# Kernel optimization log

Hardware: AMD Instinct MI355X
Metric: run time of the kernel (lower is better)

The kernel has to match this reference:

```python
import jax, jax.numpy as jnp
import numpy as np

N = 500_000      # nodes
B = 8192         # graphs
F = 128          # num_node_features
C = 128          # channels (num_out_features)
EPS = 1e-16      # matches torch_geometric.utils.softmax denominator eps


def setup_inputs() -> dict:
    key = jax.random.key(0)
    ks = jax.random.split(key, 16)
    w = lambda k, shape: jax.random.normal(k, shape, dtype=jnp.float32) * 0.02
    inp = {
        "x": jax.random.normal(ks[0], (N, F), dtype=jnp.float32),
        "u": jax.random.normal(ks[1], (B, C), dtype=jnp.float32),
        "batch": jnp.sort(jax.random.randint(ks[2], (N,), 0, B, dtype=jnp.int32)),
        "size": B,
        # gate_nn: Linear(C,C) -> ReLU -> Linear(C,1)
        "gate_w1": w(ks[3], (C, C)), "gate_b1": w(ks[4], (C,)),
        "gate_w2": w(ks[5], (C, 1)), "gate_b2": w(ks[6], (1,)),
        # node_nn: Linear(F,C) -> ReLU -> Linear(C,C)
        "node_w1": w(ks[7], (F, C)), "node_b1": w(ks[8], (C,)),
        "node_w2": w(ks[9], (C, C)), "node_b2": w(ks[10], (C,)),
        # ques_nn: Linear(C,C) -> ReLU -> Linear(C,C)
        "ques_w1": w(ks[11], (C, C)), "ques_b1": w(ks[12], (C,)),
        "ques_w2": w(ks[13], (C, C)), "ques_b2": w(ks[14], (C,)),
    }
    return inp


def _mlp2(x, w1, b1, w2, b2):
    return jax.nn.relu(x @ w1 + b1) @ w2 + b2


def reference(x, u, batch, size,
              gate_w1, gate_b1, gate_w2, gate_b2,
              node_w1, node_b1, node_w2, node_b2,
              ques_w1, ques_b1, ques_w2, ques_b2):
    # node features h_theta(x): [N, C]
    h = _mlp2(x, node_w1, node_b1, node_w2, node_b2)
    # question features per graph, gathered to nodes: [N, C]
    q = _mlp2(u, ques_w1, ques_b1, ques_w2, ques_b2)
    # gate scores: [N, 1]
    gate = _mlp2(q[batch] * h, gate_w1, gate_b1, gate_w2, gate_b2)
    # segment softmax over graphs (torch_geometric.utils.softmax)
    m = jax.ops.segment_max(gate, batch, num_segments=size)          # [B, 1]
    m = jnp.where(jnp.isfinite(m), m, 0.0)                            # empty segments
    e = jnp.exp(gate - m[batch])                                      # [N, 1]
    s = jax.ops.segment_sum(e, batch, num_segments=size)              # [B, 1]
    alpha = e / (s[batch] + EPS)                                      # [N, 1]
    # scatter_add pooling: [B, C]
    out = jax.ops.segment_sum(alpha * h, batch, num_segments=size)
    return out
```

## Files before the change

kernel.cpp:

```cpp
#include <hip/hip_runtime.h>
#include <math.h>

#define NN 500000
#define NB 8192
#define GMAX 16

typedef _Float16 f16x8 __attribute__((ext_vector_type(8)));
typedef __fp16 fp16x2 __attribute__((ext_vector_type(2)));
typedef float f32x4 __attribute__((ext_vector_type(4)));

__device__ inline f16x8 cvt8(float4 a, float4 b) {
    union { fp16x2 p[4]; f16x8 r; } u;
    u.p[0] = __builtin_amdgcn_cvt_pkrtz(a.x, a.y);
    u.p[1] = __builtin_amdgcn_cvt_pkrtz(a.z, a.w);
    u.p[2] = __builtin_amdgcn_cvt_pkrtz(b.x, b.y);
    u.p[3] = __builtin_amdgcn_cvt_pkrtz(b.z, b.w);
    return u.r;
}

__global__ void prep_w(const float* __restrict__ nw1, const float* __restrict__ nw2,
                       const float* __restrict__ gw1, const float* __restrict__ gw2,
                       const float* __restrict__ qw1, const float* __restrict__ qw2,
                       _Float16* __restrict__ wT1, _Float16* __restrict__ wT2,
                       _Float16* __restrict__ wTg, _Float16* __restrict__ wTq1,
                       _Float16* __restrict__ wTq2, _Float16* __restrict__ g2h) {
    int k = blockIdx.x;
    int n = threadIdx.x;
    wT1[n * 128 + k]  = (_Float16)nw1[k * 128 + n];
    wT2[n * 128 + k]  = (_Float16)nw2[k * 128 + n];
    wTg[n * 128 + k]  = (_Float16)gw1[k * 128 + n];
    wTq1[n * 128 + k] = (_Float16)qw1[k * 128 + n];
    wTq2[n * 128 + k] = (_Float16)qw2[k * 128 + n];
    if (k == 0) g2h[n] = (_Float16)gw2[n];
}

__launch_bounds__(512, 4)
__global__ void q_kernel(const float* __restrict__ u,
                         const _Float16* __restrict__ wTq1, const _Float16* __restrict__ wTq2,
                         const float* __restrict__ qb1, const float* __restrict__ qb2,
                         _Float16* __restrict__ q, float* __restrict__ Ppre, float* __restrict__ s) {
    __shared__ __align__(16) _Float16 tbuf[128][136];
    const int tid  = threadIdx.x;
    const int wave = tid >> 6;
    const int lane = tid & 63;
    const int lrow = lane & 15;
    const int quad = lane >> 4;
    const int wr   = wave >> 1;
    const int wc   = wave & 1;
    const int row0 = blockIdx.x * 128;
    const int rbase = wr * 32;

    for (int idx = tid; idx < 128 * 128; idx += 512) Ppre[(size_t)row0 * 128 + idx] = 0.f;
    if (tid < 128) s[row0 + tid] = 0.f;

    f32x4 acc[2][4];
    const f32x4 fz = {0.f, 0.f, 0.f, 0.f};
#pragma unroll
    for (int mi = 0; mi < 2; ++mi)
#pragma unroll
        for (int ci = 0; ci < 4; ++ci) acc[mi][ci] = fz;

#pragma unroll
    for (int ki = 0; ki < 4; ++ki) {
        const int k = ki * 32 + quad * 8;
        f16x8 a[2];
#pragma unroll
        for (int mi = 0; mi < 2; ++mi) {
            int r = row0 + rbase + mi * 16 + lrow;
            const float4* up = (const float4*)(u + (size_t)r * 128 + k);
            a[mi] = cvt8(up[0], up[1]);
        }
        f16x8 b[4];
#pragma unroll
        for (int ci = 0; ci < 4; ++ci)
            b[ci] = *(const f16x8*)(wTq1 + (size_t)(wc * 64 + ci * 16 + lrow) * 128 + k);
#pragma unroll
        for (int mi = 0; mi < 2; ++mi)
#pragma unroll
            for (int ci = 0; ci < 4; ++ci)
                acc[mi][ci] = __builtin_amdgcn_mfma_f32_16x16x32_f16(a[mi], b[ci], acc[mi][ci], 0, 0, 0);
    }
#pragma unroll
    for (int ci = 0; ci < 4; ++ci) {
        int c = wc * 64 + ci * 16 + lrow;
        float bv = qb1[c];
#pragma unroll
        for (int mi = 0; mi < 2; ++mi)
#pragma unroll
            for (int i = 0; i < 4; ++i) {
                int r = rbase + mi * 16 + quad * 4 + i;
                tbuf[r][c] = (_Float16)fmaxf(acc[mi][ci][i] + bv, 0.f);
            }
    }
    __syncthreads();

#pragma unroll
    for (int mi = 0; mi < 2; ++mi)
#pragma unroll
        for (int ci = 0; ci < 4; ++ci) acc[mi][ci] = fz;
#pragma unroll
    for (int ki = 0; ki < 4; ++ki) {
        const int k = ki * 32 + quad * 8;
        f16x8 a[2];
#pragma unroll
        for (int mi = 0; mi < 2; ++mi)
            a[mi] = *(const f16x8*)&tbuf[rbase + mi * 16 + lrow][k];
        f16x8 b[4];
#pragma unroll
        for (int ci = 0; ci < 4; ++ci)
            b[ci] = *(const f16x8*)(wTq2 + (size_t)(wc * 64 + ci * 16 + lrow) * 128 + k);
#pragma unroll
        for (int mi = 0; mi < 2; ++mi)
#pragma unroll
            for (int ci = 0; ci < 4; ++ci)
                acc[mi][ci] = __builtin_amdgcn_mfma_f32_16x16x32_f16(a[mi], b[ci], acc[mi][ci], 0, 0, 0);
    }
#pragma unroll
    for (int ci = 0; ci < 4; ++ci) {
        int c = wc * 64 + ci * 16 + lrow;
        float bv = qb2[c];
#pragma unroll
        for (int mi = 0; mi < 2; ++mi)
#pragma unroll
            for (int i = 0; i < 4; ++i) {
                int r = row0 + rbase + mi * 16 + quad * 4 + i;
                q[(size_t)r * 128 + c] = (_Float16)(acc[mi][ci][i] + bv);
            }
    }
}

__launch_bounds__(256, 4)
__global__ void hg_kernel(const float* __restrict__ x, const int* __restrict__ batch,
                          const _Float16* __restrict__ qglob,
                          const _Float16* __restrict__ wT1, const _Float16* __restrict__ wT2,
                          const _Float16* __restrict__ wTg, const _Float16* __restrict__ g2h,
                          const float* __restrict__ nb1, const float* __restrict__ nb2,
                          const float* __restrict__ gb1, const float* __restrict__ gb2,
                          float* __restrict__ Ppre, float* __restrict__ s) {
    __shared__ __align__(16) _Float16 t1buf[64][136];
    __shared__ __align__(16) _Float16 scratch[64][136];
    __shared__ __align__(16) _Float16 qsE[GMAX][136];
    __shared__ float gpart[2][64];
    __shared__ float sacc[GMAX];
    __shared__ int batch_t[64];
    __shared__ int maxrel_sh;

    const int tid  = threadIdx.x;
    const int wave = tid >> 6;
    const int lane = tid & 63;
    const int lrow = lane & 15;
    const int quad = lane >> 4;
    const int wr   = wave >> 1;
    const int wc   = wave & 1;
    const int row0 = blockIdx.x * 64;
    const int rbase = wr * 32;

    float4 xraw[4][2][2];
#pragma unroll
    for (int ki = 0; ki < 4; ++ki)
#pragma unroll
        for (int mi = 0; mi < 2; ++mi) {
            int r = min(row0 + rbase + mi * 16 + lrow, NN - 1);
            const float4* xp = (const float4*)(x + (size_t)r * 128 + ki * 32 + quad * 8);
            xraw[ki][mi][0] = xp[0];
            xraw[ki][mi][1] = xp[1];
        }

    if (wave == 0) {
        int bv = batch[min(row0 + lane, NN - 1)];
        batch_t[lane] = bv;
        int b0 = __shfl(bv, 0, 64);
        int rel = bv - b0;
#pragma unroll
        for (int off = 32; off >= 1; off >>= 1) rel = max(rel, __shfl_xor(rel, off, 64));
        if (lane == 0) maxrel_sh = rel;
    }
    __syncthreads();
    const int b_lo = batch_t[0];
    const int gcnt = min(maxrel_sh + 1, GMAX);

    for (int idx = tid; idx < gcnt * 16; idx += 256)
        *(f16x8*)&qsE[idx >> 4][(idx & 15) * 8] =
            *(const f16x8*)(qglob + (size_t)(b_lo + (idx >> 4)) * 128 + (idx & 15) * 8);

    int grel[2][4];
#pragma unroll
    for (int mi = 0; mi < 2; ++mi)
#pragma unroll
        for (int i = 0; i < 4; ++i)
            grel[mi][i] = batch_t[rbase + mi * 16 + quad * 4 + i] - b_lo;

    f16x8 a16[4][2];
#pragma unroll
    for (int ki = 0; ki < 4; ++ki)
#pragma unroll
        for (int mi = 0; mi < 2; ++mi)
            a16[ki][mi] = cvt8(xraw[ki][mi][0], xraw[ki][mi][1]);

    f32x4 acc[2][4];
    const f32x4 fz = {0.f, 0.f, 0.f, 0.f};
#pragma unroll
    for (int mi = 0; mi < 2; ++mi)
#pragma unroll
        for (int ci = 0; ci < 4; ++ci) acc[mi][ci] = fz;

#pragma unroll
    for (int ki = 0; ki < 4; ++ki) {
        const int k = ki * 32 + quad * 8;
        f16x8 b[4];
#pragma unroll
        for (int ci = 0; ci < 4; ++ci)
            b[ci] = *(const f16x8*)(wT1 + (size_t)(wc * 64 + ci * 16 + lrow) * 128 + k);
#pragma unroll
        for (int mi = 0; mi < 2; ++mi)
#pragma unroll
            for (int ci = 0; ci < 4; ++ci)
                acc[mi][ci] = __builtin_amdgcn_mfma_f32_16x16x32_f16(a16[ki][mi], b[ci], acc[mi][ci], 0, 0, 0);
    }
#pragma unroll
    for (int ci = 0; ci < 4; ++ci) {
        int c = wc * 64 + ci * 16 + lrow;
        float bv = nb1[c];
#pragma unroll
        for (int mi = 0; mi < 2; ++mi)
#pragma unroll
            for (int i = 0; i < 4; ++i) {
                int r = rbase + mi * 16 + quad * 4 + i;
                t1buf[r][c] = (_Float16)fmaxf(acc[mi][ci][i] + bv, 0.f);
            }
    }
    __syncthreads();

#pragma unroll
    for (int mi = 0; mi < 2; ++mi)
#pragma unroll
        for (int ci = 0; ci < 4; ++ci) acc[mi][ci] = fz;
#pragma unroll
    for (int ki = 0; ki < 4; ++ki) {
        const int k = ki * 32 + quad * 8;
        f16x8 a[2];
#pragma unroll
        for (int mi = 0; mi < 2; ++mi)
            a[mi] = *(const f16x8*)&t1buf[rbase + mi * 16 + lrow][k];
        f16x8 b[4];
#pragma unroll
        for (int ci = 0; ci < 4; ++ci)
            b[ci] = *(const f16x8*)(wT2 + (size_t)(wc * 64 + ci * 16 + lrow) * 128 + k);
#pragma unroll
        for (int mi = 0; mi < 2; ++mi)
#pragma unroll
            for (int ci = 0; ci < 4; ++ci)
                acc[mi][ci] = __builtin_amdgcn_mfma_f32_16x16x32_f16(a[mi], b[ci], acc[mi][ci], 0, 0, 0);
    }
#pragma unroll
    for (int ci = 0; ci < 4; ++ci) {
        int c = wc * 64 + ci * 16 + lrow;
        float bv = nb2[c];
#pragma unroll
        for (int mi = 0; mi < 2; ++mi)
#pragma unroll
            for (int i = 0; i < 4; ++i) {
                int r = rbase + mi * 16 + quad * 4 + i;
                float h = acc[mi][ci][i] + bv;
                int g = grel[mi][i];
                float qv = (g < GMAX) ? (float)qsE[g][c]
                                      : (float)qglob[(size_t)(b_lo + g) * 128 + c];
                scratch[r][c] = (_Float16)(qv * h);
            }
    }
    __syncthreads();

    for (int idx = tid; idx < GMAX * 136 / 2; idx += 256) ((float*)qsE)[idx] = 0.f;
    if (tid < GMAX) sacc[tid] = 0.f;

#pragma unroll
    for (int mi = 0; mi < 2; ++mi)
#pragma unroll
        for (int ci = 0; ci < 4; ++ci) acc[mi][ci] = fz;
    float g2hreg[4];
#pragma unroll
    for (int ci = 0; ci < 4; ++ci) g2hreg[ci] = (float)g2h[wc * 64 + ci * 16 + lrow];
#pragma unroll
    for (int ki = 0; ki < 4; ++ki) {
        const int k = ki * 32 + quad * 8;
        f16x8 a[2];
#pragma unroll
        for (int mi = 0; mi < 2; ++mi)
            a[mi] = *(const f16x8*)&scratch[rbase + mi * 16 + lrow][k];
        f16x8 b[4];
#pragma unroll
        for (int ci = 0; ci < 4; ++ci)
            b[ci] = *(const f16x8*)(wTg + (size_t)(wc * 64 + ci * 16 + lrow) * 128 + k);
#pragma unroll
        for (int mi = 0; mi < 2; ++mi)
#pragma unroll
            for (int ci = 0; ci < 4; ++ci)
                acc[mi][ci] = __builtin_amdgcn_mfma_f32_16x16x32_f16(a[mi], b[ci], acc[mi][ci], 0, 0, 0);
    }
    float p[2][4] = {{0.f, 0.f, 0.f, 0.f}, {0.f, 0.f, 0.f, 0.f}};
#pragma unroll
    for (int ci = 0; ci < 4; ++ci) {
        int c = wc * 64 + ci * 16 + lrow;
        float bv = gb1[c];
        float w = g2hreg[ci];
#pragma unroll
        for (int mi = 0; mi < 2; ++mi)
#pragma unroll
            for (int i = 0; i < 4; ++i)
                p[mi][i] = fmaf(fmaxf(acc[mi][ci][i] + bv, 0.f), w, p[mi][i]);
    }
#pragma unroll
    for (int off = 1; off <= 8; off <<= 1)
#pragma unroll
        for (int mi = 0; mi < 2; ++mi)
#pragma unroll
            for (int i = 0; i < 4; ++i)
                p[mi][i] += __shfl_xor(p[mi][i], off, 64);
    if (lrow == 0) {
#pragma unroll
        for (int mi = 0; mi < 2; ++mi)
#pragma unroll
            for (int i = 0; i < 4; ++i)
                gpart[wc][rbase + mi * 16 + quad * 4 + i] = p[mi][i];
    }
    __syncthreads();

    const float gb2v = gb2[0];
    if (tid < 64) {
        int r = tid;
        int g = batch_t[r] - b_lo;
        bool valid = (row0 + r) < NN;
        float e = valid ? __expf(gpart[0][r] + gpart[1][r] + gb2v) : 0.f;
        if (g < GMAX) {
            qsE[g][r] = (_Float16)e;
            atomicAdd(&sacc[g], e);
        } else if (valid) {
            atomicAdd(&s[b_lo + g], e);
            for (int c = 0; c < 128; ++c)
                atomicAdd(&Ppre[(size_t)(b_lo + g) * 128 + c], e * (float)t1buf[r][c]);
        }
    }
    __syncthreads();

    f16x8 aE[2];
#pragma unroll
    for (int ki = 0; ki < 2; ++ki)
        aE[ki] = *(const f16x8*)&qsE[lrow][ki * 32 + quad * 8];
    f32x4 pacc[2] = {fz, fz};
#pragma unroll
    for (int ci2 = 0; ci2 < 2; ++ci2) {
        int col = wave * 32 + ci2 * 16 + lrow;
#pragma unroll
        for (int ki = 0; ki < 2; ++ki) {
            f16x8 bh;
#pragma unroll
            for (int j = 0; j < 8; ++j) bh[j] = t1buf[ki * 32 + quad * 8 + j][col];
            pacc[ci2] = __builtin_amdgcn_mfma_f32_16x16x32_f16(aE[ki], bh, pacc[ci2], 0, 0, 0);
        }
    }
#pragma unroll
    for (int ci2 = 0; ci2 < 2; ++ci2)
#pragma unroll
        for (int i = 0; i < 4; ++i) {
            int g = quad * 4 + i;
            if (g < gcnt)
                atomicAdd(&Ppre[(size_t)(b_lo + g) * 128 + wave * 32 + ci2 * 16 + lrow], pacc[ci2][i]);
        }
    if (tid < gcnt) atomicAdd(&s[b_lo + tid], sacc[tid]);
}

__launch_bounds__(512, 4)
__global__ void fin_kernel(const float* __restrict__ Ppre, const float* __restrict__ s,
                           const _Float16* __restrict__ wT2, const float* __restrict__ nb2,
                           float* __restrict__ out) {
    const int tid  = threadIdx.x;
    const int wave = tid >> 6;
    const int lane = tid & 63;
    const int lrow = lane & 15;
    const int quad = lane >> 4;
    const int wr   = wave >> 1;
    const int wc   = wave & 1;
    const int row0 = blockIdx.x * 128;
    const int rbase = wr * 32;

    f32x4 acc[2][4];
    const f32x4 fz = {0.f, 0.f, 0.f, 0.f};
#pragma unroll
    for (int mi = 0; mi < 2; ++mi)
#pragma unroll
        for (int ci = 0; ci < 4; ++ci) acc[mi][ci] = fz;
#pragma unroll
    for (int ki = 0; ki < 4; ++ki) {
        const int k = ki * 32 + quad * 8;
        f16x8 a[2];
#pragma unroll
        for (int mi = 0; mi < 2; ++mi) {
            int r = row0 + rbase + mi * 16 + lrow;
            const float4* pp = (const float4*)(Ppre + (size_t)r * 128 + k);
            a[mi] = cvt8(pp[0], pp[1]);
        }
        f16x8 b[4];
#pragma unroll
        for (int ci = 0; ci < 4; ++ci)
            b[ci] = *(const f16x8*)(wT2 + (size_t)(wc * 64 + ci * 16 + lrow) * 128 + k);
#pragma unroll
        for (int mi = 0; mi < 2; ++mi)
#pragma unroll
            for (int ci = 0; ci < 4; ++ci)
                acc[mi][ci] = __builtin_amdgcn_mfma_f32_16x16x32_f16(a[mi], b[ci], acc[mi][ci], 0, 0, 0);
    }
    float sv[2][4], rinv[2][4];
#pragma unroll
    for (int mi = 0; mi < 2; ++mi)
#pragma unroll
        for (int i = 0; i < 4; ++i) {
            int r = row0 + rbase + mi * 16 + quad * 4 + i;
            sv[mi][i] = s[r];
            rinv[mi][i] = 1.f / (sv[mi][i] + 1e-16f);
        }
#pragma unroll
    for (int ci = 0; ci < 4; ++ci) {
        int c = wc * 64 + ci * 16 + lrow;
        float bv = nb2[c];
#pragma unroll
        for (int mi = 0; mi < 2; ++mi)
#pragma unroll
            for (int i = 0; i < 4; ++i) {
                int r = row0 + rbase + mi * 16 + quad * 4 + i;
                out[(size_t)r * 128 + c] = (acc[mi][ci][i] + sv[mi][i] * bv) * rinv[mi][i];
            }
    }
}

extern "C" void kernel_launch(void* const* d_in, const int* in_sizes, int n_in,
                              void* d_out, int out_size, void* d_ws, size_t ws_size,
                              hipStream_t stream) {
    const float* x    = (const float*)d_in[0];
    const float* u    = (const float*)d_in[1];
    const int* batch  = (const int*)d_in[2];
    const float* gw1  = (const float*)d_in[4];
    const float* gb1  = (const float*)d_in[5];
    const float* gw2  = (const float*)d_in[6];
    const float* gb2  = (const float*)d_in[7];
    const float* nw1  = (const float*)d_in[8];
    const float* nb1  = (const float*)d_in[9];
    const float* nw2  = (const float*)d_in[10];
    const float* nb2  = (const float*)d_in[11];
    const float* qw1  = (const float*)d_in[12];
    const float* qb1  = (const float*)d_in[13];
    const float* qw2  = (const float*)d_in[14];
    const float* qb2  = (const float*)d_in[15];

    char* ws = (char*)d_ws;
    _Float16* q   = (_Float16*)ws;
    float* Ppre   = (float*)(ws + 2097152);
    float* s      = (float*)(ws + 6291456);
    _Float16* wT1 = (_Float16*)(ws + 6324224);
    _Float16* wT2  = wT1 + 16384;
    _Float16* wTg  = wT2 + 16384;
    _Float16* wTq1 = wTg + 16384;
    _Float16* wTq2 = wTq1 + 16384;
    _Float16* g2h  = wTq2 + 16384;
    float* out = (float*)d_out;

    hipLaunchKernelGGL(prep_w, dim3(128), dim3(128), 0, stream,
                       nw1, nw2, gw1, gw2, qw1, qw2, wT1, wT2, wTg, wTq1, wTq2, g2h);
    hipLaunchKernelGGL(q_kernel, dim3(NB / 128), dim3(512), 0, stream,
                       u, wTq1, wTq2, qb1, qb2, q, Ppre, s);
    hipLaunchKernelGGL(hg_kernel, dim3((NN + 63) / 64), dim3(256), 0, stream,
                       x, batch, q, wT1, wT2, wTg, g2h, nb1, nb2, gb1, gb2, Ppre, s);
    hipLaunchKernelGGL(fin_kernel, dim3(NB / 128), dim3(512), 0, stream,
                       Ppre, s, wT2, nb2, out);
}
```

Baseline: 555.5 us.

## Make hg_kernel persistent and prefetch next tile's x and batch

Launches hg_kernel on a fixed grid of 1024 blocks that loop over the 64-row tiles with a grid stride, instead of one block per tile. Inside the loop, the next tile's x rows are loaded into registers, and wave 0 reads its batch ids, while the current tile's MLP, gating and pooling run. This is meant to hide global-load latency behind MFMA work and to cut block launch overhead. The cost is fewer resident blocks, so less latency hiding from occupancy, plus extra live registers for the prefetched data.

Result: slower. 890.8 us (+60.4%).

```diff
diff --git a/kernel.cpp b/kernel.cpp
--- a/kernel.cpp
+++ b/kernel.cpp
@@ -4,6 +4,8 @@
 #define NN 500000
 #define NB 8192
 #define GMAX 16
+#define HG_GRID 1024
+#define HG_NT ((NN + 63) / 64)
 
 typedef _Float16 f16x8 __attribute__((ext_vector_type(8)));
 typedef __fp16 fp16x2 __attribute__((ext_vector_type(2)));
@@ -152,221 +154,246 @@
     const int quad = lane >> 4;
     const int wr   = wave >> 1;
     const int wc   = wave & 1;
-    const int row0 = blockIdx.x * 64;
     const int rbase = wr * 32;
+    const int blk  = (int)blockIdx.x;
+
+    const f32x4 fz = {0.f, 0.f, 0.f, 0.f};
 
     float4 xraw[4][2][2];
-#pragma unroll
-    for (int ki = 0; ki < 4; ++ki)
-#pragma unroll
-        for (int mi = 0; mi < 2; ++mi) {
-            int r = min(row0 + rbase + mi * 16 + lrow, NN - 1);
-            const float4* xp = (const float4*)(x + (size_t)r * 128 + ki * 32 + quad * 8);
-            xraw[ki][mi][0] = xp[0];
-            xraw[ki][mi][1] = xp[1];
-        }
-
+    {
+        const int r0 = blk * 64;
+#pragma unroll
+        for (int ki = 0; ki < 4; ++ki)
+#pragma unroll
+            for (int mi = 0; mi < 2; ++mi) {
+                int r = min(r0 + rbase + mi * 16 + lrow, NN - 1);
+                const float4* xp = (const float4*)(x + (size_t)r * 128 + ki * 32 + quad * 8);
+                xraw[ki][mi][0] = xp[0];
+                xraw[ki][mi][1] = xp[1];
+            }
+    }
+    int bv = 0;
     if (wave == 0) {
-        int bv = batch[min(row0 + lane, NN - 1)];
-        batch_t[lane] = bv;
-        int b0 = __shfl(bv, 0, 64);
-        int rel = bv - b0;
-#pragma unroll
-        for (int off = 32; off >= 1; off >>= 1) rel = max(rel, __shfl_xor(rel, off, 64));
-        if (lane == 0) maxrel_sh = rel;
-    }
-    __syncthreads();
-    const int b_lo = batch_t[0];
-    const int gcnt = min(maxrel_sh + 1, GMAX);
-
-    for (int idx = tid; idx < gcnt * 16; idx += 256)
-        *(f16x8*)&qsE[idx >> 4][(idx & 15) * 8] =
-            *(const f16x8*)(qglob + (size_t)(b_lo + (idx >> 4)) * 128 + (idx & 15) * 8);
-
-    int grel[2][4];
-#pragma unroll
-    for (int mi = 0; mi < 2; ++mi)
-#pragma unroll
-        for (int i = 0; i < 4; ++i)
-            grel[mi][i] = batch_t[rbase + mi * 16 + quad * 4 + i] - b_lo;
-
-    f16x8 a16[4][2];
-#pragma unroll
-    for (int ki = 0; ki < 4; ++ki)
-#pragma unroll
-        for (int mi = 0; mi < 2; ++mi)
-            a16[ki][mi] = cvt8(xraw[ki][mi][0], xraw[ki][mi][1]);
-
-    f32x4 acc[2][4];
-    const f32x4 fz = {0.f, 0.f, 0.f, 0.f};
-#pragma unroll
-    for (int mi = 0; mi < 2; ++mi)
-#pragma unroll
-        for (int ci = 0; ci < 4; ++ci) acc[mi][ci] = fz;
-
-#pragma unroll
-    for (int ki = 0; ki < 4; ++ki) {
-        const int k = ki * 32 + quad * 8;
-        f16x8 b[4];
-#pragma unroll
-        for (int ci = 0; ci < 4; ++ci)
-            b[ci] = *(const f16x8*)(wT1 + (size_t)(wc * 64 + ci * 16 + lrow) * 128 + k);
-#pragma unroll
-        for (int mi = 0; mi < 2; ++mi)
+        int i0 = blk * 64 + lane;
+        bv = batch[min(i0, NN - 1)];
+    }
+
+    for (int t = blk; t < HG_NT; t += HG_GRID) {
+        const int row0  = t * 64;
+        const int rown0 = (t + HG_GRID) * 64;
+
+        if (wave == 0) {
+            batch_t[lane] = bv;
+            int b0 = __shfl(bv, 0, 64);
+            int rel = bv - b0;
+#pragma unroll
+            for (int off = 32; off >= 1; off >>= 1) rel = max(rel, __shfl_xor(rel, off, 64));
+            if (lane == 0) maxrel_sh = rel;
+        }
+        __syncthreads();
+        const int b_lo = batch_t[0];
+        const int gcnt = min(maxrel_sh + 1, GMAX);
+
+        if (wave == 0) bv = batch[min(rown0 + lane, NN - 1)];
+
+        for (int idx = tid; idx < gcnt * 16; idx += 256)
+            *(f16x8*)&qsE[idx >> 4][(idx & 15) * 8] =
+                *(const f16x8*)(qglob + (size_t)(b_lo + (idx >> 4)) * 128 + (idx & 15) * 8);
+
+        int grel[2][4];
+#pragma unroll
+        for (int mi = 0; mi < 2; ++mi)
+#pragma unroll
+            for (int i = 0; i < 4; ++i)
+                grel[mi][i] = batch_t[rbase + mi * 16 + quad * 4 + i] - b_lo;
+
+        f16x8 a16[4][2];
+#pragma unroll
+        for (int ki = 0; ki < 4; ++ki)
+#pragma unroll
+            for (int mi = 0; mi < 2; ++mi)
+                a16[ki][mi] = cvt8(xraw[ki][mi][0], xraw[ki][mi][1]);
+
+        f32x4 acc[2][4];
+#pragma unroll
+        for (int mi = 0; mi < 2; ++mi)
+#pragma unroll
+            for (int ci = 0; ci < 4; ++ci) acc[mi][ci] = fz;
+
+#pragma unroll
+        for (int ki = 0; ki < 4; ++ki) {
+            const int k = ki * 32 + quad * 8;
+            f16x8 b[4];
 #pragma unroll
             for (int ci = 0; ci < 4; ++ci)
-                acc[mi][ci] = __builtin_amdgcn_mfma_f32_16x16x32_f16(a16[ki][mi], b[ci], acc[mi][ci], 0, 0, 0);
-    }
-#pragma unroll
-    for (int ci = 0; ci < 4; ++ci) {
-        int c = wc * 64 + ci * 16 + lrow;
-        float bv = nb1[c];
-#pragma unroll
-        for (int mi = 0; mi < 2; ++mi)
+                b[ci] = *(const f16x8*)(wT1 + (size_t)(wc * 64 + ci * 16 + lrow) * 128 + k);
+#pragma unroll
+            for (int mi = 0; mi < 2; ++mi)
+#pragma unroll
+                for (int ci = 0; ci < 4; ++ci)
+                    acc[mi][ci] = __builtin_amdgcn_mfma_f32_16x16x32_f16(a16[ki][mi], b[ci], acc[mi][ci], 0, 0, 0);
+        }
+#pragma unroll
+        for (int ci = 0; ci < 4; ++ci) {
+            int c = wc * 64 + ci * 16 + lrow;
+            float bvv = nb1[c];
+#pragma unroll
+            for (int mi = 0; mi < 2; ++mi)
+#pragma unroll
+                for (int i = 0; i < 4; ++i) {
+                    int r = rbase + mi * 16 + quad * 4 + i;
+                    t1buf[r][c] = (_Float16)fmaxf(acc[mi][ci][i] + bvv, 0.f);
+                }
+        }
+        __syncthreads();
+
+#pragma unroll
+        for (int ki = 0; ki < 4; ++ki)
+#pragma unroll
+            for (int mi = 0; mi < 2; ++mi) {
+                int r = min(rown0 + rbase + mi * 16 + lrow, NN - 1);
+                const float4* xp = (const float4*)(x + (size_t)r * 128 + ki * 32 + quad * 8);
+                xraw[ki][mi][0] = xp[0];
+                xraw[ki][mi][1] = xp[1];
+            }
+
+#pragma unroll
+        for (int mi = 0; mi < 2; ++mi)
+#pragma unroll
+            for (int ci = 0; ci < 4; ++ci) acc[mi][ci] = fz;
+#pragma unroll
+        for (int ki = 0; ki < 4; ++ki) {
+            const int k = ki * 32 + quad * 8;
+            f16x8 a[2];
+#pragma unroll
+            for (int mi = 0; mi < 2; ++mi)
+                a[mi] = *(const f16x8*)&t1buf[rbase + mi * 16 + lrow][k];
+            f16x8 b[4];
+#pragma unroll
+            for (int ci = 0; ci < 4; ++ci)
+                b[ci] = *(const f16x8*)(wT2 + (size_t)(wc * 64 + ci * 16 + lrow) * 128 + k);
+#pragma unroll
+            for (int mi = 0; mi < 2; ++mi)
+#pragma unroll
+                for (int ci = 0; ci < 4; ++ci)
+                    acc[mi][ci] = __builtin_amdgcn_mfma_f32_16x16x32_f16(a[mi], b[ci], acc[mi][ci], 0, 0, 0);
+        }
+#pragma unroll
+        for (int ci = 0; ci < 4; ++ci) {
+            int c = wc * 64 + ci * 16 + lrow;
+            float bvv = nb2[c];
+#pragma unroll
+            for (int mi = 0; mi < 2; ++mi)
+#pragma unroll
+                for (int i = 0; i < 4; ++i) {
+                    int r = rbase + mi * 16 + quad * 4 + i;
+                    float h = acc[mi][ci][i] + bvv;
+                    int g = grel[mi][i];
+                    float qv = (g < GMAX) ? (float)qsE[g][c]
+                                          : (float)qglob[(size_t)(b_lo + g) * 128 + c];
+                    scratch[r][c] = (_Float16)(qv * h);
+                }
+        }
+        __syncthreads();
+
+        for (int idx = tid; idx < GMAX * 136 / 2; idx += 256) ((float*)qsE)[idx] = 0.f;
+        if (tid < GMAX) sacc[tid] = 0.f;
+
+#pragma unroll
+        for (int mi = 0; mi < 2; ++mi)
+#pragma unroll
+            for (int ci = 0; ci < 4; ++ci) acc[mi][ci] = fz;
+        float g2hreg[4];
+#pragma unroll
+        for (int ci = 0; ci < 4; ++ci) g2hreg[ci] = (float)g2h[wc * 64 + ci * 16 + lrow];
+#pragma unroll
+        for (int ki = 0; ki < 4; ++ki) {
+            const int k = ki * 32 + quad * 8;
+            f16x8 a[2];
+#pragma unroll
+            for (int mi = 0; mi < 2; ++mi)
+                a[mi] = *(const f16x8*)&scratch[rbase + mi * 16 + lrow][k];
+            f16x8 b[4];
+#pragma unroll
+            for (int ci = 0; ci < 4; ++ci)
+                b[ci] = *(const f16x8*)(wTg + (size_t)(wc * 64 + ci * 16 + lrow) * 128 + k);
+#pragma unroll
+            for (int mi = 0; mi < 2; ++mi)
+#pragma unroll
+                for (int ci = 0; ci < 4; ++ci)
+                    acc[mi][ci] = __builtin_amdgcn_mfma_f32_16x16x32_f16(a[mi], b[ci], acc[mi][ci], 0, 0, 0);
+        }
+        float p[2][4] = {{0.f, 0.f, 0.f, 0.f}, {0.f, 0.f, 0.f, 0.f}};
+#pragma unroll
+        for (int ci = 0; ci < 4; ++ci) {
+            int c = wc * 64 + ci * 16 + lrow;
+            float bvv = gb1[c];
+            float w = g2hreg[ci];
+#pragma unroll
+            for (int mi = 0; mi < 2; ++mi)
+#pragma unroll
+                for (int i = 0; i < 4; ++i)
+                    p[mi][i] = fmaf(fmaxf(acc[mi][ci][i] + bvv, 0.f), w, p[mi][i]);
+        }
+#pragma unroll
+        for (int off = 1; off <= 8; off <<= 1)
+#pragma unroll
+            for (int mi = 0; mi < 2; ++mi)
+#pragma unroll
+                for (int i = 0; i < 4; ++i)
+                    p[mi][i] += __shfl_xor(p[mi][i], off, 64);
+        if (lrow == 0) {
+#pragma unroll
+            for (int mi = 0; mi < 2; ++mi)
+#pragma unroll
+                for (int i = 0; i < 4; ++i)
+                    gpart[wc][rbase + mi * 16 + quad * 4 + i] = p[mi][i];
+        }
+        __syncthreads();
+
+        const float gb2v = gb2[0];
+        if (tid < 64) {
+            int r = tid;
+            int g = batch_t[r] - b_lo;
+            bool valid = (row0 + r) < NN;
+            float e = valid ? __expf(gpart[0][r] + gpart[1][r] + gb2v) : 0.f;
+            if (g < GMAX) {
+                qsE[g][r] = (_Float16)e;
+                atomicAdd(&sacc[g], e);
+            } else if (valid) {
+                atomicAdd(&s[b_lo + g], e);
+                for (int c = 0; c < 128; ++c)
+                    atomicAdd(&Ppre[(size_t)(b_lo + g) * 128 + c], e * (float)t1buf[r][c]);
+            }
+        }
+        __syncthreads();
+
+        f16x8 aE[2];
+#pragma unroll
+        for (int ki = 0; ki < 2; ++ki)
+            aE[ki] = *(const f16x8*)&qsE[lrow][ki * 32 + quad * 8];
+        f32x4 pacc[2] = {fz, fz};
+#pragma unroll
+        for (int ci2 = 0; ci2 < 2; ++ci2) {
+            int col = wave * 32 + ci2 * 16 + lrow;
+#pragma unroll
+            for (int ki = 0; ki < 2; ++ki) {
+                f16x8 bh;
+#pragma unroll
+                for (int j = 0; j < 8; ++j) bh[j] = t1buf[ki * 32 + quad * 8 + j][col];
+                pacc[ci2] = __builtin_amdgcn_mfma_f32_16x16x32_f16(aE[ki], bh, pacc[ci2], 0, 0, 0);
+            }
+        }
+#pragma unroll
+        for (int ci2 = 0; ci2 < 2; ++ci2)
 #pragma unroll
             for (int i = 0; i < 4; ++i) {
-                int r = rbase + mi * 16 + quad * 4 + i;
-                t1buf[r][c] = (_Float16)fmaxf(acc[mi][ci][i] + bv, 0.f);
-            }
-    }
-    __syncthreads();
-
-#pragma unroll
-    for (int mi = 0; mi < 2; ++mi)
-#pragma unroll
-        for (int ci = 0; ci < 4; ++ci) acc[mi][ci] = fz;
-#pragma unroll
-    for (int ki = 0; ki < 4; ++ki) {
-        const int k = ki * 32 + quad * 8;
-        f16x8 a[2];
-#pragma unroll
-        for (int mi = 0; mi < 2; ++mi)
-            a[mi] = *(const f16x8*)&t1buf[rbase + mi * 16 + lrow][k];
-        f16x8 b[4];
-#pragma unroll
-        for (int ci = 0; ci < 4; ++ci)
-            b[ci] = *(const f16x8*)(wT2 + (size_t)(wc * 64 + ci * 16 + lrow) * 128 + k);
-#pragma unroll
-        for (int mi = 0; mi < 2; ++mi)
-#pragma unroll
-            for (int ci = 0; ci < 4; ++ci)
-                acc[mi][ci] = __builtin_amdgcn_mfma_f32_16x16x32_f16(a[mi], b[ci], acc[mi][ci], 0, 0, 0);
-    }
-#pragma unroll
-    for (int ci = 0; ci < 4; ++ci) {
-        int c = wc * 64 + ci * 16 + lrow;
-        float bv = nb2[c];
-#pragma unroll
-        for (int mi = 0; mi < 2; ++mi)
-#pragma unroll
-            for (int i = 0; i < 4; ++i) {
-                int r = rbase + mi * 16 + quad * 4 + i;
-                float h = acc[mi][ci][i] + bv;
-                int g = grel[mi][i];
-                float qv = (g < GMAX) ? (float)qsE[g][c]
-                                      : (float)qglob[(size_t)(b_lo + g) * 128 + c];
-                scratch[r][c] = (_Float16)(qv * h);
-            }
-    }
-    __syncthreads();
-
-    for (int idx = tid; idx < GMAX * 136 / 2; idx += 256) ((float*)qsE)[idx] = 0.f;
-    if (tid < GMAX) sacc[tid] = 0.f;
-
-#pragma unroll
-    for (int mi = 0; mi < 2; ++mi)
-#pragma unroll
-        for (int ci = 0; ci < 4; ++ci) acc[mi][ci] = fz;
-    float g2hreg[4];
-#pragma unroll
-    for (int ci = 0; ci < 4; ++ci) g2hreg[ci] = (float)g2h[wc * 64 + ci * 16 + lrow];
-#pragma unroll
-    for (int ki = 0; ki < 4; ++ki) {
-        const int k = ki * 32 + quad * 8;
-        f16x8 a[2];
-#pragma unroll
-        for (int mi = 0; mi < 2; ++mi)
-            a[mi] = *(const f16x8*)&scratch[rbase + mi * 16 + lrow][k];
-        f16x8 b[4];
-#pragma unroll
-        for (int ci = 0; ci < 4; ++ci)
-            b[ci] = *(const f16x8*)(wTg + (size_t)(wc * 64 + ci * 16 + lrow) * 128 + k);
-#pragma unroll
-        for (int mi = 0; mi < 2; ++mi)
-#pragma unroll
-            for (int ci = 0; ci < 4; ++ci)
-                acc[mi][ci] = __builtin_amdgcn_mfma_f32_16x16x32_f16(a[mi], b[ci], acc[mi][ci], 0, 0, 0);
-    }
-    float p[2][4] = {{0.f, 0.f, 0.f, 0.f}, {0.f, 0.f, 0.f, 0.f}};
-#pragma unroll
-    for (int ci = 0; ci < 4; ++ci) {
-        int c = wc * 64 + ci * 16 + lrow;
-        float bv = gb1[c];
-        float w = g2hreg[ci];
-#pragma unroll
-        for (int mi = 0; mi < 2; ++mi)
-#pragma unroll
-            for (int i = 0; i < 4; ++i)
-                p[mi][i] = fmaf(fmaxf(acc[mi][ci][i] + bv, 0.f), w, p[mi][i]);
-    }
-#pragma unroll
-    for (int off = 1; off <= 8; off <<= 1)
-#pragma unroll
-        for (int mi = 0; mi < 2; ++mi)
-#pragma unroll
-            for (int i = 0; i < 4; ++i)
-                p[mi][i] += __shfl_xor(p[mi][i], off, 64);
-    if (lrow == 0) {
-#pragma unroll
-        for (int mi = 0; mi < 2; ++mi)
-#pragma unroll
-            for (int i = 0; i < 4; ++i)
-                gpart[wc][rbase + mi * 16 + quad * 4 + i] = p[mi][i];
-    }
-    __syncthreads();
-
-    const float gb2v = gb2[0];
-    if (tid < 64) {
-        int r = tid;
-        int g = batch_t[r] - b_lo;
-        bool valid = (row0 + r) < NN;
-        float e = valid ? __expf(gpart[0][r] + gpart[1][r] + gb2v) : 0.f;
-        if (g < GMAX) {
-            qsE[g][r] = (_Float16)e;
-            atomicAdd(&sacc[g], e);
-        } else if (valid) {
-            atomicAdd(&s[b_lo + g], e);
-            for (int c = 0; c < 128; ++c)
-                atomicAdd(&Ppre[(size_t)(b_lo + g) * 128 + c], e * (float)t1buf[r][c]);
-        }
-    }
-    __syncthreads();
-
-    f16x8 aE[2];
-#pragma unroll
-    for (int ki = 0; ki < 2; ++ki)
-        aE[ki] = *(const f16x8*)&qsE[lrow][ki * 32 + quad * 8];
-    f32x4 pacc[2] = {fz, fz};
-#pragma unroll
-    for (int ci2 = 0; ci2 < 2; ++ci2) {
-        int col = wave * 32 + ci2 * 16 + lrow;
-#pragma unroll
-        for (int ki = 0; ki < 2; ++ki) {
-            f16x8 bh;
-#pragma unroll
-            for (int j = 0; j < 8; ++j) bh[j] = t1buf[ki * 32 + quad * 8 + j][col];
-            pacc[ci2] = __builtin_amdgcn_mfma_f32_16x16x32_f16(aE[ki], bh, pacc[ci2], 0, 0, 0);
-        }
-    }
-#pragma unroll
-    for (int ci2 = 0; ci2 < 2; ++ci2)
-#pragma unroll
-        for (int i = 0; i < 4; ++i) {
-            int g = quad * 4 + i;
-            if (g < gcnt)
-                atomicAdd(&Ppre[(size_t)(b_lo + g) * 128 + wave * 32 + ci2 * 16 + lrow], pacc[ci2][i]);
-        }
-    if (tid < gcnt) atomicAdd(&s[b_lo + tid], sacc[tid]);
+                int g = quad * 4 + i;
+                if (g < gcnt)
+                    atomicAdd(&Ppre[(size_t)(b_lo + g) * 128 + wave * 32 + ci2 * 16 + lrow], pacc[ci2][i]);
+            }
+        if (tid < gcnt) atomicAdd(&s[b_lo + tid], sacc[tid]);
+    }
 }
 
 __launch_bounds__(512, 4)
@@ -467,7 +494,7 @@
                        nw1, nw2, gw1, gw2, qw1, qw2, wT1, wT2, wTg, wTq1, wTq2, g2h);
     hipLaunchKernelGGL(q_kernel, dim3(NB / 128), dim3(512), 0, stream,
                        u, wTq1, wTq2, qb1, qb2, q, Ppre, s);
-    hipLaunchKernelGGL(hg_kernel, dim3((NN + 63) / 64), dim3(256), 0, stream,
+    hipLaunchKernelGGL(hg_kernel, dim3(HG_GRID), dim3(256), 0, stream,
                        x, batch, q, wT1, wT2, wTg, g2h, nb1, nb2, gb1, gb2, Ppre, s);
     hipLaunchKernelGGL(fin_kernel, dim3(NB / 128), dim3(512), 0, stream,
                        Ppre, s, wT2, nb2, out);
```

## Make hg_kernel persistent with prefetch of next tile and double-buffered LDS

Applied to the files above, without the earlier changes.

Converts hg_kernel into a persistent grid-stride loop over 64-row tiles with a fixed grid of 1536 blocks. The x and batch data for the next tile are prefetched into registers while the current tile computes, and the t1/E buffers are double-buffered so a single barrier per tile suffices. Each wave now owns 16 full rows across all 128 columns instead of a 2x2 wave split. q rows are read straight from global memory instead of being staged in shared memory, and the segment sums are computed from the E buffer. The aim is to hide HBM latency and cut barrier and launch overhead, at the cost of higher register pressure (launch bounds lowered to 1) and lower occupancy.

After: 598.4 us. +7.7%, slower.

```diff
diff --git a/kernel.cpp b/kernel.cpp
--- a/kernel.cpp
+++ b/kernel.cpp
@@ -4,6 +4,8 @@
 #define NN 500000
 #define NB 8192
 #define GMAX 16
+#define HG_GRID 1536
+#define HG_NT ((NN + 63) / 64)
 
 typedef _Float16 f16x8 __attribute__((ext_vector_type(8)));
 typedef __fp16 fp16x2 __attribute__((ext_vector_type(2)));
@@ -129,7 +131,7 @@
     }
 }
 
-__launch_bounds__(256, 4)
+__launch_bounds__(256, 1)
 __global__ void hg_kernel(const float* __restrict__ x, const int* __restrict__ batch,
                           const _Float16* __restrict__ qglob,
                           const _Float16* __restrict__ wT1, const _Float16* __restrict__ wT2,
@@ -137,236 +139,208 @@
                           const float* __restrict__ nb1, const float* __restrict__ nb2,
                           const float* __restrict__ gb1, const float* __restrict__ gb2,
                           float* __restrict__ Ppre, float* __restrict__ s) {
-    __shared__ __align__(16) _Float16 t1buf[64][136];
+    __shared__ __align__(16) _Float16 t1buf[2][64][136];
+    __shared__ __align__(16) _Float16 Ebuf[2][GMAX][136];
     __shared__ __align__(16) _Float16 scratch[64][136];
-    __shared__ __align__(16) _Float16 qsE[GMAX][136];
-    __shared__ float gpart[2][64];
-    __shared__ float sacc[GMAX];
-    __shared__ int batch_t[64];
-    __shared__ int maxrel_sh;
 
     const int tid  = threadIdx.x;
     const int wave = tid >> 6;
     const int lane = tid & 63;
     const int lrow = lane & 15;
     const int quad = lane >> 4;
-    const int wr   = wave >> 1;
-    const int wc   = wave & 1;
-    const int row0 = blockIdx.x * 64;
-    const int rbase = wr * 32;
-
-    float4 xraw[4][2][2];
-#pragma unroll
-    for (int ki = 0; ki < 4; ++ki)
-#pragma unroll
-        for (int mi = 0; mi < 2; ++mi) {
-            int r = min(row0 + rbase + mi * 16 + lrow, NN - 1);
-            const float4* xp = (const float4*)(x + (size_t)r * 128 + ki * 32 + quad * 8);
-            xraw[ki][mi][0] = xp[0];
-            xraw[ki][mi][1] = xp[1];
-        }
-
-    if (wave == 0) {
-        int bv = batch[min(row0 + lane, NN - 1)];
-        batch_t[lane] = bv;
-        int b0 = __shfl(bv, 0, 64);
-        int rel = bv - b0;
+    const int rbase = wave * 16;
+    const int blk  = (int)blockIdx.x;
+    const f32x4 fz = {0.f, 0.f, 0.f, 0.f};
+
+    f16x8 a16[4];
+    {
+        int r = min(blk * 64 + rbase + lrow, NN - 1);
+        const float4* xp = (const float4*)(x + (size_t)r * 128 + quad * 8);
+#pragma unroll
+        for (int ki = 0; ki < 4; ++ki)
+            a16[ki] = cvt8(xp[ki * 8], xp[ki * 8 + 1]);
+    }
+    int bv = batch[min(blk * 64 + lane, NN - 1)];
+
+    int pb = 0;
+    for (int t = blk; t < HG_NT; t += HG_GRID, pb ^= 1) {
+        const int row0  = t * 64;
+        const int rown0 = (t + HG_GRID) * 64;
+
+        const int b_lo = __shfl(bv, 0, 64);
+        int rel = bv - b_lo;
 #pragma unroll
         for (int off = 32; off >= 1; off >>= 1) rel = max(rel, __shfl_xor(rel, off, 64));
-        if (lane == 0) maxrel_sh = rel;
-    }
-    __syncthreads();
-    const int b_lo = batch_t[0];
-    const int gcnt = min(maxrel_sh + 1, GMAX);
-
-    for (int idx = tid; idx < gcnt * 16; idx += 256)
-        *(f16x8*)&qsE[idx >> 4][(idx & 15) * 8] =
-            *(const f16x8*)(qglob + (size_t)(b_lo + (idx >> 4)) * 128 + (idx & 15) * 8);
-
-    int grel[2][4];
-#pragma unroll
-    for (int mi = 0; mi < 2; ++mi)
+        const int gcnt = min(rel + 1, GMAX);
+        int gown[4];
 #pragma unroll
         for (int i = 0; i < 4; ++i)
-            grel[mi][i] = batch_t[rbase + mi * 16 + quad * 4 + i] - b_lo;
-
-    f16x8 a16[4][2];
-#pragma unroll
-    for (int ki = 0; ki < 4; ++ki)
-#pragma unroll
-        for (int mi = 0; mi < 2; ++mi)
-            a16[ki][mi] = cvt8(xraw[ki][mi][0], xraw[ki][mi][1]);
-
-    f32x4 acc[2][4];
-    const f32x4 fz = {0.f, 0.f, 0.f, 0.f};
-#pragma unroll
-    for (int mi = 0; mi < 2; ++mi)
-#pragma unroll
-        for (int ci = 0; ci < 4; ++ci) acc[mi][ci] = fz;
-
-#pragma unroll
-    for (int ki = 0; ki < 4; ++ki) {
-        const int k = ki * 32 + quad * 8;
-        f16x8 b[4];
-#pragma unroll
-        for (int ci = 0; ci < 4; ++ci)
-            b[ci] = *(const f16x8*)(wT1 + (size_t)(wc * 64 + ci * 16 + lrow) * 128 + k);
-#pragma unroll
-        for (int mi = 0; mi < 2; ++mi)
-#pragma unroll
-            for (int ci = 0; ci < 4; ++ci)
-                acc[mi][ci] = __builtin_amdgcn_mfma_f32_16x16x32_f16(a16[ki][mi], b[ci], acc[mi][ci], 0, 0, 0);
-    }
-#pragma unroll
-    for (int ci = 0; ci < 4; ++ci) {
-        int c = wc * 64 + ci * 16 + lrow;
-        float bv = nb1[c];
-#pragma unroll
-        for (int mi = 0; mi < 2; ++mi)
+            gown[i] = __shfl(bv, rbase + quad * 4 + i, 64) - b_lo;
+        int bv_next = batch[min(rown0 + lane, NN - 1)];
+
+        {
+            int g  = lane >> 2;
+            int rr = (lane & 3) * 4;
+            *(float2*)&Ebuf[pb][g][rbase + rr] = make_float2(0.f, 0.f);
+        }
+
+        f32x4 acc[8];
+#pragma unroll
+        for (int ci = 0; ci < 8; ++ci) acc[ci] = fz;
+#pragma unroll
+        for (int ki = 0; ki < 4; ++ki) {
+            const int k = ki * 32 + quad * 8;
+            f16x8 b[8];
+#pragma unroll
+            for (int ci = 0; ci < 8; ++ci)
+                b[ci] = *(const f16x8*)(wT1 + (size_t)(ci * 16 + lrow) * 128 + k);
+#pragma unroll
+            for (int ci = 0; ci < 8; ++ci)
+                acc[ci] = __builtin_amdgcn_mfma_f32_16x16x32_f16(a16[ki], b[ci], acc[ci], 0, 0, 0);
+        }
+#pragma unroll
+        for (int ci = 0; ci < 8; ++ci) {
+            int c = ci * 16 + lrow;
+            float bv1 = nb1[c];
+#pragma unroll
+            for (int i = 0; i < 4; ++i)
+                t1buf[pb][rbase + quad * 4 + i][c] = (_Float16)fmaxf(acc[ci][i] + bv1, 0.f);
+        }
+
+        __builtin_amdgcn_sched_barrier(0);
+        float4 xraw[4][2];
+        {
+            int r = min(rown0 + rbase + lrow, NN - 1);
+            const float4* xp = (const float4*)(x + (size_t)r * 128 + quad * 8);
+#pragma unroll
+            for (int ki = 0; ki < 4; ++ki) {
+                xraw[ki][0] = xp[ki * 8];
+                xraw[ki][1] = xp[ki * 8 + 1];
+            }
+        }
+
+#pragma unroll
+        for (int ci = 0; ci < 8; ++ci) acc[ci] = fz;
+#pragma unroll
+        for (int ki = 0; ki < 4; ++ki) {
+            const int k = ki * 32 + quad * 8;
+            f16x8 a = *(const f16x8*)&t1buf[pb][rbase + lrow][k];
+            f16x8 b[8];
+#pragma unroll
+            for (int ci = 0; ci < 8; ++ci)
+                b[ci] = *(const f16x8*)(wT2 + (size_t)(ci * 16 + lrow) * 128 + k);
+#pragma unroll
+            for (int ci = 0; ci < 8; ++ci)
+                acc[ci] = __builtin_amdgcn_mfma_f32_16x16x32_f16(a, b[ci], acc[ci], 0, 0, 0);
+        }
+        {
+            float nb2c[8];
+#pragma unroll
+            for (int ci = 0; ci < 8; ++ci) nb2c[ci] = nb2[ci * 16 + lrow];
 #pragma unroll
             for (int i = 0; i < 4; ++i) {
-                int r = rbase + mi * 16 + quad * 4 + i;
-                t1buf[r][c] = (_Float16)fmaxf(acc[mi][ci][i] + bv, 0.f);
-            }
-    }
-    __syncthreads();
-
-#pragma unroll
-    for (int mi = 0; mi < 2; ++mi)
-#pragma unroll
-        for (int ci = 0; ci < 4; ++ci) acc[mi][ci] = fz;
-#pragma unroll
-    for (int ki = 0; ki < 4; ++ki) {
-        const int k = ki * 32 + quad * 8;
-        f16x8 a[2];
-#pragma unroll
-        for (int mi = 0; mi < 2; ++mi)
-            a[mi] = *(const f16x8*)&t1buf[rbase + mi * 16 + lrow][k];
-        f16x8 b[4];
-#pragma unroll
-        for (int ci = 0; ci < 4; ++ci)
-            b[ci] = *(const f16x8*)(wT2 + (size_t)(wc * 64 + ci * 16 + lrow) * 128 + k);
-#pragma unroll
-        for (int mi = 0; mi < 2; ++mi)
-#pragma unroll
-            for (int ci = 0; ci < 4; ++ci)
-                acc[mi][ci] = __builtin_amdgcn_mfma_f32_16x16x32_f16(a[mi], b[ci], acc[mi][ci], 0, 0, 0);
-    }
-#pragma unroll
-    for (int ci = 0; ci < 4; ++ci) {
-        int c = wc * 64 + ci * 16 + lrow;
-        float bv = nb2[c];
-#pragma unroll
-        for (int mi = 0; mi < 2; ++mi)
+                const _Float16* qrow = qglob + (size_t)(b_lo + gown[i]) * 128;
+                int r = rbase + quad * 4 + i;
+#pragma unroll
+                for (int ci = 0; ci < 8; ++ci) {
+                    int c = ci * 16 + lrow;
+                    float h = acc[ci][i] + nb2c[ci];
+                    scratch[r][c] = (_Float16)((float)qrow[c] * h);
+                }
+            }
+        }
+
+#pragma unroll
+        for (int ci = 0; ci < 8; ++ci) acc[ci] = fz;
+#pragma unroll
+        for (int ki = 0; ki < 4; ++ki) {
+            const int k = ki * 32 + quad * 8;
+            f16x8 a = *(const f16x8*)&scratch[rbase + lrow][k];
+            f16x8 b[8];
+#pragma unroll
+            for (int ci = 0; ci < 8; ++ci)
+                b[ci] = *(const f16x8*)(wTg + (size_t)(ci * 16 + lrow) * 128 + k);
+#pragma unroll
+            for (int ci = 0; ci < 8; ++ci)
+                acc[ci] = __builtin_amdgcn_mfma_f32_16x16x32_f16(a, b[ci], acc[ci], 0, 0, 0);
+        }
+        {
+            float p[4] = {0.f, 0.f, 0.f, 0.f};
+#pragma unroll
+            for (int ci = 0; ci < 8; ++ci) {
+                int c = ci * 16 + lrow;
+                float b1 = gb1[c];
+                float w = (float)g2h[c];
+#pragma unroll
+                for (int i = 0; i < 4; ++i)
+                    p[i] = fmaf(fmaxf(acc[ci][i] + b1, 0.f), w, p[i]);
+            }
+#pragma unroll
+            for (int off = 1; off <= 8; off <<= 1)
+#pragma unroll
+                for (int i = 0; i < 4; ++i)
+                    p[i] += __shfl_xor(p[i], off, 64);
+            const float gb2v = gb2[0];
+            if (lrow == 0) {
+#pragma unroll
+                for (int i = 0; i < 4; ++i) {
+                    int r = rbase + quad * 4 + i;
+                    bool valid = (row0 + r) < NN;
+                    float e = valid ? __expf(p[i] + gb2v) : 0.f;
+                    int g = gown[i];
+                    if (g < GMAX) {
+                        Ebuf[pb][g][r] = (_Float16)e;
+                    } else if (valid) {
+                        atomicAdd(&s[b_lo + g], e);
+                        for (int c = 0; c < 128; ++c)
+                            atomicAdd(&Ppre[(size_t)(b_lo + g) * 128 + c],
+                                      e * (float)t1buf[pb][r][c]);
+                    }
+                }
+            }
+        }
+
+#pragma unroll
+        for (int ki = 0; ki < 4; ++ki)
+            a16[ki] = cvt8(xraw[ki][0], xraw[ki][1]);
+        bv = bv_next;
+
+        __syncthreads();
+
+        f16x8 aE[2];
+#pragma unroll
+        for (int ki2 = 0; ki2 < 2; ++ki2)
+            aE[ki2] = *(const f16x8*)&Ebuf[pb][lrow][ki2 * 32 + quad * 8];
+        f32x4 pacc[2] = {fz, fz};
+#pragma unroll
+        for (int ci2 = 0; ci2 < 2; ++ci2) {
+            int col = wave * 32 + ci2 * 16 + lrow;
+#pragma unroll
+            for (int ki2 = 0; ki2 < 2; ++ki2) {
+                f16x8 bh;
+#pragma unroll
+                for (int j = 0; j < 8; ++j) bh[j] = t1buf[pb][ki2 * 32 + quad * 8 + j][col];
+                pacc[ci2] = __builtin_amdgcn_mfma_f32_16x16x32_f16(aE[ki2], bh, pacc[ci2], 0, 0, 0);
+            }
+        }
+#pragma unroll
+        for (int ci2 = 0; ci2 < 2; ++ci2)
 #pragma unroll
             for (int i = 0; i < 4; ++i) {
-                int r = rbase + mi * 16 + quad * 4 + i;
-                float h = acc[mi][ci][i] + bv;
-                int g = grel[mi][i];
-                float qv = (g < GMAX) ? (float)qsE[g][c]
-                                      : (float)qglob[(size_t)(b_lo + g) * 128 + c];
-                scratch[r][c] = (_Float16)(qv * h);
-            }
-    }
-    __syncthreads();
-
-    for (int idx = tid; idx < GMAX * 136 / 2; idx += 256) ((float*)qsE)[idx] = 0.f;
-    if (tid < GMAX) sacc[tid] = 0.f;
-
-#pragma unroll
-    for (int mi = 0; mi < 2; ++mi)
-#pragma unroll
-        for (int ci = 0; ci < 4; ++ci) acc[mi][ci] = fz;
-    float g2hreg[4];
-#pragma unroll
-    for (int ci = 0; ci < 4; ++ci) g2hreg[ci] = (float)g2h[wc * 64 + ci * 16 + lrow];
-#pragma unroll
-    for (int ki = 0; ki < 4; ++ki) {
-        const int k = ki * 32 + quad * 8;
-        f16x8 a[2];
-#pragma unroll
-        for (int mi = 0; mi < 2; ++mi)
-            a[mi] = *(const f16x8*)&scratch[rbase + mi * 16 + lrow][k];
-        f16x8 b[4];
-#pragma unroll
-        for (int ci = 0; ci < 4; ++ci)
-            b[ci] = *(const f16x8*)(wTg + (size_t)(wc * 64 + ci * 16 + lrow) * 128 + k);
-#pragma unroll
-        for (int mi = 0; mi < 2; ++mi)
-#pragma unroll
-            for (int ci = 0; ci < 4; ++ci)
-                acc[mi][ci] = __builtin_amdgcn_mfma_f32_16x16x32_f16(a[mi], b[ci], acc[mi][ci], 0, 0, 0);
-    }
-    float p[2][4] = {{0.f, 0.f, 0.f, 0.f}, {0.f, 0.f, 0.f, 0.f}};
-#pragma unroll
-    for (int ci = 0; ci < 4; ++ci) {
-        int c = wc * 64 + ci * 16 + lrow;
-        float bv = gb1[c];
-        float w = g2hreg[ci];
-#pragma unroll
-        for (int mi = 0; mi < 2; ++mi)
-#pragma unroll
-            for (int i = 0; i < 4; ++i)
-                p[mi][i] = fmaf(fmaxf(acc[mi][ci][i] + bv, 0.f), w, p[mi][i]);
-    }
-#pragma unroll
-    for (int off = 1; off <= 8; off <<= 1)
-#pragma unroll
-        for (int mi = 0; mi < 2; ++mi)
-#pragma unroll
-            for (int i = 0; i < 4; ++i)
-                p[mi][i] += __shfl_xor(p[mi][i], off, 64);
-    if (lrow == 0) {
-#pragma unroll
-        for (int mi = 0; mi < 2; ++mi)
-#pragma unroll
-            for (int i = 0; i < 4; ++i)
-                gpart[wc][rbase + mi * 16 + quad * 4 + i] = p[mi][i];
-    }
-    __syncthreads();
-
-    const float gb2v = gb2[0];
-    if (tid < 64) {
-        int r = tid;
-        int g = batch_t[r] - b_lo;
-        bool valid = (row0 + r) < NN;
-        float e = valid ? __expf(gpart[0][r] + gpart[1][r] + gb2v) : 0.f;
-        if (g < GMAX) {
-            qsE[g][r] = (_Float16)e;
-            atomicAdd(&sacc[g], e);
-        } else if (valid) {
-            atomicAdd(&s[b_lo + g], e);
-            for (int c = 0; c < 128; ++c)
-                atomicAdd(&Ppre[(size_t)(b_lo + g) * 128 + c], e * (float)t1buf[r][c]);
-        }
-    }
-    __syncthreads();
-
-    f16x8 aE[2];
-#pragma unroll
-    for (int ki = 0; ki < 2; ++ki)
-        aE[ki] = *(const f16x8*)&qsE[lrow][ki * 32 + quad * 8];
-    f32x4 pacc[2] = {fz, fz};
-#pragma unroll
-    for (int ci2 = 0; ci2 < 2; ++ci2) {
-        int col = wave * 32 + ci2 * 16 + lrow;
-#pragma unroll
-        for (int ki = 0; ki < 2; ++ki) {
-            f16x8 bh;
-#pragma unroll
-            for (int j = 0; j < 8; ++j) bh[j] = t1buf[ki * 32 + quad * 8 + j][col];
-            pacc[ci2] = __builtin_amdgcn_mfma_f32_16x16x32_f16(aE[ki], bh, pacc[ci2], 0, 0, 0);
-        }
-    }
-#pragma unroll
-    for (int ci2 = 0; ci2 < 2; ++ci2)
-#pragma unroll
-        for (int i = 0; i < 4; ++i) {
-            int g = quad * 4 + i;
-            if (g < gcnt)
-                atomicAdd(&Ppre[(size_t)(b_lo + g) * 128 + wave * 32 + ci2 * 16 + lrow], pacc[ci2][i]);
-        }
-    if (tid < gcnt) atomicAdd(&s[b_lo + tid], sacc[tid]);
+                int g = quad * 4 + i;
+                if (g < gcnt)
+                    atomicAdd(&Ppre[(size_t)(b_lo + g) * 128 + wave * 32 + ci2 * 16 + lrow],
+                              pacc[ci2][i]);
+            }
+        if (wave == 0) {
+            float sv = 0.f;
+#pragma unroll
+            for (int j = 0; j < 16; ++j) sv += (float)Ebuf[pb][lrow][quad * 16 + j];
+            sv += __shfl_xor(sv, 16, 64);
+            sv += __shfl_xor(sv, 32, 64);
+            if (quad == 0 && lrow < gcnt) atomicAdd(&s[b_lo + lrow], sv);
+        }
+    }
 }
 
 __launch_bounds__(512, 4)
@@ -467,7 +441,7 @@
                        nw1, nw2, gw1, gw2, qw1, qw2, wT1, wT2, wTg, wTq1, wTq2, g2h);
     hipLaunchKernelGGL(q_kernel, dim3(NB / 128), dim3(512), 0, stream,
                        u, wTq1, wTq2, qb1, qb2, q, Ppre, s);
-    hipLaunchKernelGGL(hg_kernel, dim3((NN + 63) / 64), dim3(256), 0, stream,
+    hipLaunchKernelGGL(hg_kernel, dim3(HG_GRID), dim3(256), 0, stream,
                        x, batch, q, wT1, wT2, wTg, g2h, nb1, nb2, gb1, gb2, Ppre, s);
     hipLaunchKernelGGL(fin_kernel, dim3(NB / 128), dim3(512), 0, stream,
                        Ppre, s, wT2, nb2, out);
```
